# Kernel tuning notes

Measured on AMD Instinct MI355X. Metric: run time of the kernel, lower is better.

## Reference

```python
import jax, jax.numpy as jnp
import numpy as np

N_U, N_M, E, L = 100000, 20000, 2000000, 500000
F_U, F_M, H = 64, 128, 128


def setup_inputs() -> dict:
    key = jax.random.key(0)
    ks = jax.random.split(key, 48)
    p = lambda k, shape: jax.random.normal(k, shape, jnp.float32) * 0.02
    inp = {
        'x_user': jax.random.normal(ks[0], (N_U, F_U), jnp.float32),
        'x_movie': jax.random.normal(ks[1], (N_M, F_M), jnp.float32),
        'edge_index': jnp.stack([jax.random.randint(ks[2], (E,), 0, N_U),
                                 jax.random.randint(ks[3], (E,), 0, N_M)]),
        'edge_label_index': jnp.stack([jax.random.randint(ks[4], (L,), 0, N_U),
                                       jax.random.randint(ks[5], (L,), 0, N_M)]),
        # per-type input projections (LazyLinear)
        'lin_u_W': p(ks[6], (H, F_U)), 'lin_u_b': p(ks[7], (H,)),
        'lin_m_W': p(ks[8], (H, F_M)), 'lin_m_b': p(ks[9], (H,)),
        # BatchNorm (eval mode: running stats)
        'bn_u_g': 1.0 + p(ks[10], (H,)), 'bn_u_b': p(ks[11], (H,)),
        'bn_u_m': p(ks[12], (H,)) * 5.0,
        'bn_u_v': jax.random.uniform(ks[13], (H,), jnp.float32, 0.5, 1.5),
        'bn_m_g': 1.0 + p(ks[14], (H,)), 'bn_m_b': p(ks[15], (H,)),
        'bn_m_m': p(ks[16], (H,)) * 5.0,
        'bn_m_v': jax.random.uniform(ks[17], (H,), jnp.float32, 0.5, 1.5),
        # conv1: SAGEConv per relation (Wl applied to aggregated, Wr to root)
        'c1_um_Wl': p(ks[18], (H, H)), 'c1_um_bl': p(ks[19], (H,)), 'c1_um_Wr': p(ks[20], (H, H)),
        'c1_mu_Wl': p(ks[21], (H, H)), 'c1_mu_bl': p(ks[22], (H,)), 'c1_mu_Wr': p(ks[23], (H, H)),
        # conv2
        'c2_um_Wl': p(ks[24], (H, H)), 'c2_um_bl': p(ks[25], (H,)), 'c2_um_Wr': p(ks[26], (H, H)),
        'c2_mu_Wl': p(ks[27], (H, H)), 'c2_mu_bl': p(ks[28], (H,)), 'c2_mu_Wr': p(ks[29], (H, H)),
        # edge decoder MLP: 2H -> 4H -> 2H -> 1
        'dec_W1': p(ks[30], (4 * H, 2 * H)), 'dec_b1': p(ks[31], (4 * H,)),
        'dec_W2': p(ks[32], (2 * H, 4 * H)), 'dec_b2': p(ks[33], (2 * H,)),
        'dec_W3': p(ks[34], (1, 2 * H)), 'dec_b3': p(ks[35], (1,)),
    }
    return inp


def _bn(x, g, b, m, v):
    return (x - m) * jax.lax.rsqrt(v + 1e-5) * g + b


def _seg_mean(msg, dst, n):
    s = jax.ops.segment_sum(msg, dst, num_segments=n)
    c = jax.ops.segment_sum(jnp.ones((dst.shape[0], 1), msg.dtype), dst, num_segments=n)
    return s / jnp.maximum(c, 1.0)


def _sage(x_src, x_dst, src, dst, Wl, bl, Wr):
    # PyG SAGEConv(aggr='mean'): lin_l(mean of source msgs) + lin_r(x_dst)
    agg = _seg_mean(x_src[src], dst, x_dst.shape[0])
    return agg @ Wl.T + bl + x_dst @ Wr.T


def reference(x_user, x_movie, edge_index, edge_label_index,
              lin_u_W, lin_u_b, lin_m_W, lin_m_b,
              bn_u_g, bn_u_b, bn_u_m, bn_u_v,
              bn_m_g, bn_m_b, bn_m_m, bn_m_v,
              c1_um_Wl, c1_um_bl, c1_um_Wr, c1_mu_Wl, c1_mu_bl, c1_mu_Wr,
              c2_um_Wl, c2_um_bl, c2_um_Wr, c2_mu_Wl, c2_mu_bl, c2_mu_Wr,
              dec_W1, dec_b1, dec_W2, dec_b2, dec_W3, dec_b3):
    u, m = edge_index[0], edge_index[1]
    # per-type projection + BN(eval) + ReLU (Dropout is identity in eval)
    xu = jnp.maximum(_bn(x_user @ lin_u_W.T + lin_u_b, bn_u_g, bn_u_b, bn_u_m, bn_u_v), 0.0)
    xm = jnp.maximum(_bn(x_movie @ lin_m_W.T + lin_m_b, bn_m_g, bn_m_b, bn_m_m, bn_m_v), 0.0)
    # conv1: user->movie and movie->user (HeteroConv mean over 1 relation each)
    xm1 = jnp.maximum(_sage(xu, xm, u, m, c1_um_Wl, c1_um_bl, c1_um_Wr), 0.0)
    xu1 = jnp.maximum(_sage(xm, xu, m, u, c1_mu_Wl, c1_mu_bl, c1_mu_Wr), 0.0)
    # conv2 (no activation after, matches forward)
    zm = _sage(xu1, xm1, u, m, c2_um_Wl, c2_um_bl, c2_um_Wr)
    zu = _sage(xm1, xu1, m, u, c2_mu_Wl, c2_mu_bl, c2_mu_Wr)
    # edge decoder: gather + MLP
    feat = jnp.concatenate([zu[edge_label_index[0]], zm[edge_label_index[1]]], axis=-1)
    h = jnp.maximum(feat @ dec_W1.T + dec_b1, 0.0)
    h = jnp.maximum(h @ dec_W2.T + dec_b2, 0.0)
    return (h @ dec_W3.T + dec_b3)[:, 0]
```

## Files before the change

### kernel.cpp

```cpp
#include <hip/hip_runtime.h>

#define NU 100000
#define NM 20000
#define NE 2000000
#define NL 500000
#define H  128
#define MROW 48

typedef __attribute__((ext_vector_type(8))) short bf16x8;
typedef __attribute__((ext_vector_type(4))) float floatx4;
typedef __attribute__((ext_vector_type(8))) unsigned short u16x8;
typedef __attribute__((ext_vector_type(4))) unsigned short u16x4;

__device__ __forceinline__ unsigned short f2b(float x) {
    union { __bf16 h; unsigned short u; } v;
    v.h = (__bf16)x;
    return v.u;
}
__device__ __forceinline__ float b2f(unsigned short h) {
    union { unsigned u; float f; } v; v.u = ((unsigned)h) << 16;
    return v.f;
}

#define SFCH(r, c)  ((r) * 32 + (((c) + (r)) & 31))
#define SH1CH(r, c) ((r) * 16 + (((c) + (r)) & 15))
#define SH2CH(r, c) ((r) * 64 + (((c) + (r)) & 63))

struct TDesc { const float* s; float* d; int R; int C; };
struct TPack { TDesc t[2]; };

__global__ __launch_bounds__(256) void transpose_all(TPack p) {
    TDesc d = p.t[blockIdx.y];
    int n = d.R * d.C;
    for (int i = blockIdx.x * 256 + threadIdx.x; i < n; i += gridDim.x * 256) {
        int r = i / d.C, c = i - r * d.C;
        d.d[c * d.R + r] = d.s[i];
    }
}

__global__ __launch_bounds__(256) void pack_weights(const float* __restrict__ W1,
                                                    const float* __restrict__ W2,
                                                    unsigned short* __restrict__ W1p,
                                                    unsigned short* __restrict__ W2p) {
    const int n = 512 * 256;
    for (int i = blockIdx.x * 256 + threadIdx.x; i < n; i += gridDim.x * 256) {
        int j = i & 7, lane = (i >> 3) & 63;
        int ln = lane & 15, lq = lane >> 4;
        int kg1 = (i >> 9) & 7,  t1 = i >> 12;
        W1p[i] = f2b(W1[(t1 * 16 + ln) * 256 + kg1 * 32 + lq * 8 + j]);
        int kg2 = (i >> 9) & 15, t2 = i >> 13;
        W2p[i] = f2b(W2[(t2 * 16 + ln) * 512 + kg2 * 32 + lq * 8 + j]);
    }
}

struct SPack { const float* w[8]; };
__global__ __launch_bounds__(256) void pack_sage(SPack sp, unsigned short* __restrict__ out) {
    const int n = 8 * 16384;
    for (int i = blockIdx.x * 256 + threadIdx.x; i < n; i += gridDim.x * 256) {
        int j = i & 7, lane = (i >> 3) & 63;
        int kg = (i >> 9) & 3, t = (i >> 11) & 7, wsel = i >> 14;
        int ln = lane & 15, lq = lane >> 4;
        out[i] = f2b(sp.w[wsel][(t * 16 + ln) * H + kg * 32 + lq * 8 + j]);
    }
}

__global__ __launch_bounds__(256) void deg_kernel(const int* __restrict__ ei,
                                                  int* rp_m, int* rp_u) {
    for (int i = blockIdx.x * 256 + threadIdx.x; i < NE; i += gridDim.x * 256) {
        int u = ei[i], m = ei[NE + i];
        atomicAdd(&rp_u[u + 1], 1);
        atomicAdd(&rp_m[m + 1], 1);
    }
}

__global__ __launch_bounds__(256) void scan_p1(const int* __restrict__ rp_m, int n_m,
                                               const int* __restrict__ rp_u, int n_u,
                                               int* __restrict__ aux) {
    const int arr = blockIdx.y;
    const int* a = arr ? rp_u : rp_m;
    const int n  = arr ? n_u : n_m;
    const int nb = (n + 4095) >> 12;
    const int b  = blockIdx.x;
    if (b >= nb) return;
    __shared__ int s[256];
    const int tid = threadIdx.x;
    int i0 = (b << 12) + tid * 16;
    int run = 0;
#pragma unroll
    for (int i = 0; i < 16; ++i) { int idx = i0 + i; run += (idx < n) ? a[idx] : 0; }
    s[tid] = run;
    __syncthreads();
    for (int off = 128; off > 0; off >>= 1) {
        if (tid < off) s[tid] += s[tid + off];
        __syncthreads();
    }
    if (tid == 0) aux[arr * 32 + b] = s[0];
}

__global__ __launch_bounds__(256) void scan_p2(int* __restrict__ rp_m, int n_m,
                                               int* __restrict__ rp_u, int n_u,
                                               const int* __restrict__ aux) {
    const int arr = blockIdx.y;
    int* a = arr ? rp_u : rp_m;
    const int n  = arr ? n_u : n_m;
    const int nb = (n + 4095) >> 12;
    const int b  = blockIdx.x;
    if (b >= nb) return;
    __shared__ int s[256];
    __shared__ int sc;
    const int tid = threadIdx.x;
    if (tid == 0) {
        int c = 0;
        for (int i = 0; i < b; ++i) c += aux[arr * 32 + i];
        sc = c;
    }
    int i0 = (b << 12) + tid * 16;
    int v[16];
    int run = 0;
#pragma unroll
    for (int i = 0; i < 16; ++i) {
        int idx = i0 + i;
        int x = (idx < n) ? a[idx] : 0;
        run += x; v[i] = run;
    }
    s[tid] = run;
    __syncthreads();
    for (int off = 1; off < 256; off <<= 1) {
        int t = (tid >= off) ? s[tid - off] : 0;
        __syncthreads();
        s[tid] += t;
        __syncthreads();
    }
    int prev = sc + (tid > 0 ? s[tid - 1] : 0);
#pragma unroll
    for (int i = 0; i < 16; ++i) {
        int idx = i0 + i;
        if (idx < n) a[idx] = v[i] + prev;
    }
}

__global__ __launch_bounds__(256) void bucket_kernel(const int* __restrict__ ei,
        const int* __restrict__ rp_m, const int* __restrict__ rp_u,
        int* cur_m, int* cur_u, int* es_m, int* es_u) {
    for (int i = blockIdx.x * 256 + threadIdx.x; i < NE; i += gridDim.x * 256) {
        int u = ei[i], m = ei[NE + i];
        int pm = atomicAdd(&cur_m[m], 1);
        es_m[rp_m[m] + pm] = u;
        int pu = atomicAdd(&cur_u[u], 1);
        es_u[rp_u[u] + pu] = m;
    }
}

template <int K>
__global__ __launch_bounds__(256, 2) void proj_kernel(
        const float* __restrict__ x, const float* __restrict__ Wt,
        const float* __restrict__ lb, const float* __restrict__ g,
        const float* __restrict__ bb, const float* __restrict__ bm,
        const float* __restrict__ bv, unsigned short* __restrict__ out, int N) {
    __shared__ float sA[64 * K];
    const int tid = threadIdx.x;
    const int row0 = blockIdx.x * 64;
    constexpr int F4 = K / 4;
#pragma unroll
    for (int i = 0; i < (64 * F4) / 256; ++i) {
        int idx = tid + i * 256;
        int r = idx / F4, c = idx - r * F4;
        int gr = min(row0 + r, N - 1);
        ((float4*)sA)[idx] = ((const float4*)(x + (size_t)gr * K))[c];
    }
    __syncthreads();
    const int h_t = tid & 31, r_t = tid >> 5;
    float acc[8][4] = {};
#pragma unroll 4
    for (int k = 0; k < K; k += 4) {
        float4 w[4];
#pragma unroll
        for (int kk = 0; kk < 4; ++kk)
            w[kk] = *(const float4*)(Wt + (k + kk) * H + h_t * 4);
#pragma unroll
        for (int rr = 0; rr < 8; ++rr) {
            float4 a = *(const float4*)(sA + (r_t * 8 + rr) * K + k);
            acc[rr][0] += a.x * w[0].x + a.y * w[1].x + a.z * w[2].x + a.w * w[3].x;
            acc[rr][1] += a.x * w[0].y + a.y * w[1].y + a.z * w[2].y + a.w * w[3].y;
            acc[rr][2] += a.x * w[0].z + a.y * w[1].z + a.z * w[2].z + a.w * w[3].z;
            acc[rr][3] += a.x * w[0].w + a.y * w[1].w + a.z * w[2].w + a.w * w[3].w;
        }
    }
    const int h = h_t * 4;
    float4 lb4 = *(const float4*)(lb + h);
    float4 g4  = *(const float4*)(g  + h);
    float4 bb4 = *(const float4*)(bb + h);
    float4 m4  = *(const float4*)(bm + h);
    float4 v4  = *(const float4*)(bv + h);
    float sc[4] = { g4.x * rsqrtf(v4.x + 1e-5f), g4.y * rsqrtf(v4.y + 1e-5f),
                    g4.z * rsqrtf(v4.z + 1e-5f), g4.w * rsqrtf(v4.w + 1e-5f) };
    float lbv[4] = { lb4.x, lb4.y, lb4.z, lb4.w };
    float mv[4]  = { m4.x, m4.y, m4.z, m4.w };
    float bbv[4] = { bb4.x, bb4.y, bb4.z, bb4.w };
#pragma unroll
    for (int rr = 0; rr < 8; ++rr) {
        int gr = row0 + r_t * 8 + rr;
        if (gr < N) {
            u16x4 o;
#pragma unroll
            for (int c = 0; c < 4; ++c)
                o[c] = f2b(fmaxf((acc[rr][c] + lbv[c] - mv[c]) * sc[c] + bbv[c], 0.0f));
            *(u16x4*)(out + (size_t)gr * H + h) = o;
        }
    }
}

__global__ __launch_bounds__(256) void agg_bf16(
        const unsigned short* __restrict__ srcA, const int* __restrict__ esA,
        const int* __restrict__ rpA, unsigned short* __restrict__ outA, int nA,
        const unsigned short* __restrict__ srcB, const int* __restrict__ esB,
        const int* __restrict__ rpB, unsigned short* __restrict__ outB, int nB) {
    int wid = blockIdx.x * 4 + (threadIdx.x >> 6);
    const int lane = threadIdx.x & 63;
    const unsigned short* src; const int* es; const int* rp; unsigned short* out; int n;
    if (wid < nA) { src = srcA; es = esA; rp = rpA; out = outA; n = wid; }
    else {
        wid -= nA;
        if (wid >= nB) return;
        src = srcB; es = esB; rp = rpB; out = outB; n = wid;
    }
    const int start = rp[n], end = rp[n + 1];
    const int cb = (lane & 15) * 8;
    const int ro = lane >> 4;
    float acc[8] = {};
    if (end > start) {
        int j = start;
        for (; j + 16 <= end; j += 16) {
            u16x8 v0 = *(const u16x8*)(src + (size_t)es[j +      ro] * H + cb);
            u16x8 v1 = *(const u16x8*)(src + (size_t)es[j +  4 + ro] * H + cb);
            u16x8 v2 = *(const u16x8*)(src + (size_t)es[j +  8 + ro] * H + cb);
            u16x8 v3 = *(const u16x8*)(src + (size_t)es[j + 12 + ro] * H + cb);
#pragma unroll
            for (int e = 0; e < 8; ++e)
                acc[e] += b2f(v0[e]) + b2f(v1[e]) + b2f(v2[e]) + b2f(v3[e]);
        }
        for (; j + 4 <= end; j += 4) {
            u16x8 v = *(const u16x8*)(src + (size_t)es[j + ro] * H + cb);
#pragma unroll
            for (int e = 0; e < 8; ++e) acc[e] += b2f(v[e]);
        }
        if (j < end) {
            int idx = j + ro;
            int row = es[idx < end ? idx : end - 1];
            float m = (idx < end) ? 1.0f : 0.0f;
            u16x8 v = *(const u16x8*)(src + (size_t)row * H + cb);
#pragma unroll
            for (int e = 0; e < 8; ++e) acc[e] = fmaf(m, b2f(v[e]), acc[e]);
        }
    }
#pragma unroll
    for (int e = 0; e < 8; ++e) {
        acc[e] += __shfl_xor(acc[e], 16);
        acc[e] += __shfl_xor(acc[e], 32);
    }
    float inv = (end > start) ? 1.0f / (float)(end - start) : 0.0f;
    if (ro == 0) {
        u16x8 o;
#pragma unroll
        for (int e = 0; e < 8; ++e) o[e] = f2b(acc[e] * inv);
        *(u16x8*)(out + (size_t)n * H + cb) = o;
    }
}

__global__ __launch_bounds__(256, 4) void sage_mfma(
        const unsigned short* __restrict__ aggA, const unsigned short* __restrict__ xA,
        const unsigned short* __restrict__ WlA, const unsigned short* __restrict__ WrA,
        const float* __restrict__ blA, unsigned short* __restrict__ outA, int NA, int NBLKA,
        const unsigned short* __restrict__ aggB, const unsigned short* __restrict__ xB,
        const unsigned short* __restrict__ WlB, const unsigned short* __restrict__ WrB,
        const float* __restrict__ blB, unsigned short* __restrict__ outB, int NB,
        int relu) {
    __shared__ unsigned short sAg[64 * 16 * 8];
    __shared__ unsigned short sX[64 * 16 * 8];
    const int tid = threadIdx.x;
    const unsigned short *agg, *x, *Wl, *Wr; const float* bl; unsigned short* out;
    int N, row0;
    if ((int)blockIdx.x < NBLKA) {
        agg = aggA; x = xA; Wl = WlA; Wr = WrA; bl = blA; out = outA; N = NA;
        row0 = blockIdx.x * 64;
    } else {
        agg = aggB; x = xB; Wl = WlB; Wr = WrB; bl = blB; out = outB; N = NB;
        row0 = (blockIdx.x - NBLKA) * 64;
    }
#pragma unroll
    for (int i = 0; i < 4; ++i) {
        int idx = tid + i * 256;
        int r = idx >> 4, c = idx & 15;
        int gr = min(row0 + r, N - 1);
        *(u16x8*)(sAg + SH1CH(r, c) * 8) = *(const u16x8*)(agg + (size_t)gr * H + c * 8);
        *(u16x8*)(sX  + SH1CH(r, c) * 8) = *(const u16x8*)(x   + (size_t)gr * H + c * 8);
    }
    __syncthreads();
    const int lane = tid & 63, w = tid >> 6;
    const int ln = lane & 15, lq = lane >> 4;
    floatx4 acc[2][4] = {};
#pragma unroll 2
    for (int kg = 0; kg < 4; ++kg) {
        bf16x8 aA[4], aX[4];
#pragma unroll
        for (int mt = 0; mt < 4; ++mt) {
            aA[mt] = *(const bf16x8*)(sAg + SH1CH(mt * 16 + ln, kg * 4 + lq) * 8);
            aX[mt] = *(const bf16x8*)(sX  + SH1CH(mt * 16 + ln, kg * 4 + lq) * 8);
        }
#pragma unroll
        for (int nt = 0; nt < 2; ++nt) {
            int widx = ((w * 2 + nt) * 4 + kg) * 512 + lane * 8;
            bf16x8 bL = *(const bf16x8*)(Wl + widx);
            bf16x8 bR = *(const bf16x8*)(Wr + widx);
#pragma unroll
            for (int mt = 0; mt < 4; ++mt) {
                acc[nt][mt] = __builtin_amdgcn_mfma_f32_16x16x32_bf16(aA[mt], bL, acc[nt][mt], 0, 0, 0);
                acc[nt][mt] = __builtin_amdgcn_mfma_f32_16x16x32_bf16(aX[mt], bR, acc[nt][mt], 0, 0, 0);
            }
        }
    }
    __syncthreads();
    {
#pragma unroll
        for (int nt = 0; nt < 2; ++nt) {
            int ncol = w * 32 + nt * 16 + ln;
            float bv = bl[ncol];
            int cch = ncol >> 3, coff = ncol & 7;
#pragma unroll
            for (int mt = 0; mt < 4; ++mt)
#pragma unroll
                for (int i = 0; i < 4; ++i) {
                    int row = mt * 16 + lq * 4 + i;
                    float v = acc[nt][mt][i] + bv;
                    if (relu) v = fmaxf(v, 0.0f);
                    sAg[SH1CH(row, cch) * 8 + coff] = f2b(v);
                }
        }
    }
    __syncthreads();
#pragma unroll
    for (int i = 0; i < 4; ++i) {
        int idx = tid + i * 256;
        int r = idx >> 4, c = idx & 15;
        int gr = row0 + r;
        if (gr < N)
            *(u16x8*)(out + (size_t)gr * H + c * 8) = *(const u16x8*)(sAg + SH1CH(r, c) * 8);
    }
}

__global__ __launch_bounds__(512, 4) void decoder_mfma(
        const unsigned short* __restrict__ zu, const unsigned short* __restrict__ zm,
        const int* __restrict__ eli,
        const unsigned short* __restrict__ W1p, const float* __restrict__ b1,
        const unsigned short* __restrict__ W2p, const float* __restrict__ b2,
        const float* __restrict__ W3, const float* __restrict__ b3,
        float* __restrict__ out) {
    __shared__ unsigned short sF[MROW * 32 * 8];
    __shared__ unsigned short sH1[MROW * 64 * 8];
    const int tid = threadIdx.x;
    const int row0 = blockIdx.x * MROW;
    {
        int r = tid >> 3, p = tid & 7;
        if (r < MROW) {
            int rg = min(row0 + r, NL - 1);
            int iu = eli[rg], im = eli[NL + rg];
            const unsigned short* zur = zu + (size_t)iu * H;
            const unsigned short* zmr = zm + (size_t)im * H;
#pragma unroll
            for (int j = 0; j < 4; ++j) {
                int c = p + j * 8;
                const unsigned short* s = (c < 16) ? (zur + c * 8) : (zmr + (c - 16) * 8);
                *(u16x8*)(sF + SFCH(r, c) * 8) = *(const u16x8*)s;
            }
        }
    }
    __syncthreads();
    const int lane = tid & 63, w = tid >> 6;
    const int ln = lane & 15, lq = lane >> 4;
    {
        floatx4 acc1[4][3] = {};
        const unsigned short* w1base = W1p + ((size_t)(w * 4) * 8) * 512 + lane * 8;
        __builtin_amdgcn_s_setprio(1);
#pragma unroll 2
        for (int kg = 0; kg < 8; ++kg) {
            bf16x8 fb[3];
#pragma unroll
            for (int mt = 0; mt < 3; ++mt)
                fb[mt] = *(const bf16x8*)(sF + SFCH(mt * 16 + ln, kg * 4 + lq) * 8);
#pragma unroll
            for (int nt = 0; nt < 4; ++nt) {
                bf16x8 wa = *(const bf16x8*)(w1base + (size_t)(nt * 8 + kg) * 512);
#pragma unroll
                for (int mt = 0; mt < 3; ++mt)
                    acc1[nt][mt] = __builtin_amdgcn_mfma_f32_16x16x32_bf16(wa, fb[mt], acc1[nt][mt], 0, 0, 0);
            }
        }
        __builtin_amdgcn_s_setprio(0);
#pragma unroll
        for (int nt = 0; nt < 4; ++nt) {
            int colbase = w * 64 + nt * 16 + lq * 4;
            float4 bv = *(const float4*)(b1 + colbase);
            int cch = colbase >> 3, coff = colbase & 7;
#pragma unroll
            for (int mt = 0; mt < 3; ++mt) {
                int erow = mt * 16 + ln;
                u16x4 o = { f2b(fmaxf(acc1[nt][mt][0] + bv.x, 0.0f)),
                            f2b(fmaxf(acc1[nt][mt][1] + bv.y, 0.0f)),
                            f2b(fmaxf(acc1[nt][mt][2] + bv.z, 0.0f)),
                            f2b(fmaxf(acc1[nt][mt][3] + bv.w, 0.0f)) };
                *(u16x4*)(sH1 + SH2CH(erow, cch) * 8 + coff) = o;
            }
        }
    }
    __syncthreads();
    floatx4 acc3[2][3] = {};
    {
        const unsigned short* w2base = W2p + ((size_t)(w * 2) * 16) * 512 + lane * 8;
        __builtin_amdgcn_s_setprio(1);
#pragma unroll 2
        for (int kg = 0; kg < 16; ++kg) {
            bf16x8 hb[3];
#pragma unroll
            for (int mt = 0; mt < 3; ++mt)
                hb[mt] = *(const bf16x8*)(sH1 + SH2CH(mt * 16 + ln, kg * 4 + lq) * 8);
#pragma unroll
            for (int nt = 0; nt < 2; ++nt) {
                bf16x8 wa = *(const bf16x8*)(w2base + (size_t)(nt * 16 + kg) * 512);
#pragma unroll
                for (int mt = 0; mt < 3; ++mt)
                    acc3[nt][mt] = __builtin_amdgcn_mfma_f32_16x16x32_bf16(wa, hb[mt], acc3[nt][mt], 0, 0, 0);
            }
        }
        __builtin_amdgcn_s_setprio(0);
    }
    float* sP = (float*)sF;
    {
        float4 w3a = *(const float4*)(W3 + w * 32 + lq * 4);
        float4 w3b = *(const float4*)(W3 + w * 32 + 16 + lq * 4);
        float4 b2a = *(const float4*)(b2 + w * 32 + lq * 4);
        float4 b2b = *(const float4*)(b2 + w * 32 + 16 + lq * 4);
#pragma unroll
        for (int mt = 0; mt < 3; ++mt) {
            float s =
                fmaxf(acc3[0][mt][0] + b2a.x, 0.0f) * w3a.x +
                fmaxf(acc3[0][mt][1] + b2a.y, 0.0f) * w3a.y +
                fmaxf(acc3[0][mt][2] + b2a.z, 0.0f) * w3a.z +
                fmaxf(acc3[0][mt][3] + b2a.w, 0.0f) * w3a.w +
                fmaxf(acc3[1][mt][0] + b2b.x, 0.0f) * w3b.x +
                fmaxf(acc3[1][mt][1] + b2b.y, 0.0f) * w3b.y +
                fmaxf(acc3[1][mt][2] + b2b.z, 0.0f) * w3b.z +
                fmaxf(acc3[1][mt][3] + b2b.w, 0.0f) * w3b.w;
            sP[(mt * 16 + ln) * 36 + w * 4 + lq] = s;
        }
    }
    __syncthreads();
    {
        int r = tid >> 3, p = tid & 7;
        if (r < MROW) {
            float4 v = *(const float4*)(sP + r * 36 + p * 4);
            float sum = v.x + v.y + v.z + v.w;
            sum += __shfl_down(sum, 4, 8);
            sum += __shfl_down(sum, 2, 8);
            sum += __shfl_down(sum, 1, 8);
            if (p == 0 && row0 + r < NL) out[row0 + r] = sum + b3[0];
        }
    }
}

extern "C" void kernel_launch(void* const* d_in, const int* in_sizes, int n_in,
                              void* d_out, int out_size, void* d_ws, size_t ws_size,
                              hipStream_t stream) {
    const float* x_user  = (const float*)d_in[0];
    const float* x_movie = (const float*)d_in[1];
    const int*   ei      = (const int*)d_in[2];
    const int*   eli     = (const int*)d_in[3];
    const float* lin_u_W = (const float*)d_in[4];
    const float* lin_u_b = (const float*)d_in[5];
    const float* lin_m_W = (const float*)d_in[6];
    const float* lin_m_b = (const float*)d_in[7];
    const float* bn_u_g  = (const float*)d_in[8];
    const float* bn_u_b  = (const float*)d_in[9];
    const float* bn_u_m  = (const float*)d_in[10];
    const float* bn_u_v  = (const float*)d_in[11];
    const float* bn_m_g  = (const float*)d_in[12];
    const float* bn_m_b  = (const float*)d_in[13];
    const float* bn_m_m  = (const float*)d_in[14];
    const float* bn_m_v  = (const float*)d_in[15];
    const float* c1_um_Wl = (const float*)d_in[16];
    const float* c1_um_bl = (const float*)d_in[17];
    const float* c1_um_Wr = (const float*)d_in[18];
    const float* c1_mu_Wl = (const float*)d_in[19];
    const float* c1_mu_bl = (const float*)d_in[20];
    const float* c1_mu_Wr = (const float*)d_in[21];
    const float* c2_um_Wl = (const float*)d_in[22];
    const float* c2_um_bl = (const float*)d_in[23];
    const float* c2_um_Wr = (const float*)d_in[24];
    const float* c2_mu_Wl = (const float*)d_in[25];
    const float* c2_mu_bl = (const float*)d_in[26];
    const float* c2_mu_Wr = (const float*)d_in[27];
    const float* dec_W1 = (const float*)d_in[28];
    const float* dec_b1 = (const float*)d_in[29];
    const float* dec_W2 = (const float*)d_in[30];
    const float* dec_b2 = (const float*)d_in[31];
    const float* dec_W3 = (const float*)d_in[32];
    const float* dec_b3 = (const float*)d_in[33];

    char* base = (char*)d_ws;
    size_t off = 0;
    auto alloc = [&](size_t bytes) -> char* {
        char* p = base + off;
        off += (bytes + 255) & ~(size_t)255;
        return p;
    };
    unsigned short* xu_b  = (unsigned short*)alloc((size_t)NU * H * 2);
    unsigned short* xm_b  = (unsigned short*)alloc((size_t)NM * H * 2);
    unsigned short* xu1_b = (unsigned short*)alloc((size_t)NU * H * 2);
    unsigned short* xm1_b = (unsigned short*)alloc((size_t)NM * H * 2);
    unsigned short* aggu  = (unsigned short*)alloc((size_t)NU * H * 2);
    unsigned short* aggm  = (unsigned short*)alloc((size_t)NM * H * 2);
    float* wt_u = (float*)alloc((size_t)64 * H * 4);
    float* wt_m = (float*)alloc((size_t)H * H * 4);
    unsigned short* wsg = (unsigned short*)alloc((size_t)8 * 16384 * 2);
    unsigned short* w1p = (unsigned short*)alloc((size_t)512 * 256 * 2);
    unsigned short* w2p = (unsigned short*)alloc((size_t)256 * 512 * 2);
    int* rp_m  = (int*)alloc((size_t)(NM + 1) * 4);
    int* rp_u  = (int*)alloc((size_t)(NU + 1) * 4);
    int* cur_m = (int*)alloc((size_t)NM * 4);
    int* cur_u = (int*)alloc((size_t)NU * 4);
    int* es_m  = (int*)alloc((size_t)NE * 4);
    int* es_u  = (int*)alloc((size_t)NE * 4);
    int* scan_aux = (int*)alloc((size_t)64 * 4);
    unsigned short* zu = xu_b;
    unsigned short* zm = xm_b;

    hipMemsetAsync(rp_m, 0, (size_t)((char*)es_m - (char*)rp_m), stream);

    TPack tp;
    tp.t[0] = { lin_u_W, wt_u, H, 64 };
    tp.t[1] = { lin_m_W, wt_m, H, H };
    transpose_all<<<dim3(64, 2), 256, 0, stream>>>(tp);
    pack_weights<<<256, 256, 0, stream>>>(dec_W1, dec_W2, w1p, w2p);
    SPack sp;
    sp.w[0] = c1_um_Wl; sp.w[1] = c1_um_Wr; sp.w[2] = c1_mu_Wl; sp.w[3] = c1_mu_Wr;
    sp.w[4] = c2_um_Wl; sp.w[5] = c2_um_Wr; sp.w[6] = c2_mu_Wl; sp.w[7] = c2_mu_Wr;
    pack_sage<<<128, 256, 0, stream>>>(sp, wsg);
    const unsigned short* W_c1um_l = wsg + 0 * 16384;
    const unsigned short* W_c1um_r = wsg + 1 * 16384;
    const unsigned short* W_c1mu_l = wsg + 2 * 16384;
    const unsigned short* W_c1mu_r = wsg + 3 * 16384;
    const unsigned short* W_c2um_l = wsg + 4 * 16384;
    const unsigned short* W_c2um_r = wsg + 5 * 16384;
    const unsigned short* W_c2mu_l = wsg + 6 * 16384;
    const unsigned short* W_c2mu_r = wsg + 7 * 16384;

    deg_kernel<<<2048, 256, 0, stream>>>(ei, rp_m, rp_u);
    scan_p1<<<dim3(25, 2), 256, 0, stream>>>(rp_m, NM + 1, rp_u, NU + 1, scan_aux);
    scan_p2<<<dim3(25, 2), 256, 0, stream>>>(rp_m, NM + 1, rp_u, NU + 1, scan_aux);
    bucket_kernel<<<2048, 256, 0, stream>>>(ei, rp_m, rp_u, cur_m, cur_u, es_m, es_u);

    proj_kernel<64><<<(NU + 63) / 64, 256, 0, stream>>>(
        x_user, wt_u, lin_u_b, bn_u_g, bn_u_b, bn_u_m, bn_u_v, xu_b, NU);
    proj_kernel<128><<<(NM + 63) / 64, 256, 0, stream>>>(
        x_movie, wt_m, lin_m_b, bn_m_g, bn_m_b, bn_m_m, bn_m_v, xm_b, NM);

    const int AGG_BLOCKS = (NM + NU + 3) / 4;
    const int NBLK_M = (NM + 63) / 64, NBLK_U = (NU + 63) / 64;

    agg_bf16<<<AGG_BLOCKS, 256, 0, stream>>>(xu_b, es_m, rp_m, aggm, NM,
                                             xm_b, es_u, rp_u, aggu, NU);
    sage_mfma<<<NBLK_M + NBLK_U, 256, 0, stream>>>(
        aggm, xm_b, W_c1um_l, W_c1um_r, c1_um_bl, xm1_b, NM, NBLK_M,
        aggu, xu_b, W_c1mu_l, W_c1mu_r, c1_mu_bl, xu1_b, NU, 1);
    agg_bf16<<<AGG_BLOCKS, 256, 0, stream>>>(xu1_b, es_m, rp_m, aggm, NM,
                                             xm1_b, es_u, rp_u, aggu, NU);
    sage_mfma<<<NBLK_M + NBLK_U, 256, 0, stream>>>(
        aggm, xm1_b, W_c2um_l, W_c2um_r, c2_um_bl, zm, NM, NBLK_M,
        aggu, xu1_b, W_c2mu_l, W_c2mu_r, c2_mu_bl, zu, NU, 0);

    decoder_mfma<<<(NL + MROW - 1) / MROW, 512, 0, stream>>>(
        zu, zm, eli, w1p, dec_b1, w2p, dec_b2, dec_W3, dec_b3, (float*)d_out);
}
```

Baseline: 1.116 ms.

## Fuse prep kernels, record atomic slot in degree pass, merge bucket with projection

The weight transpose and packing kernels are merged with the degree-count kernel into one launch, and each edge's atomicAdd result is saved as its slot within its bucket. The bucket pass then writes edges directly using that saved slot, with no second round of atomics. It runs in the same launch as the user and movie projections. This cuts the number of kernel launches and the contended atomics, at the cost of an extra 16 MB of slot arrays stored in the aggu buffer. It also removes the s_setprio hints from the decoder MFMA loops.

```diff
diff --git a/kernel.cpp b/kernel.cpp
--- a/kernel.cpp
+++ b/kernel.cpp
@@ -26,50 +26,53 @@
 #define SH1CH(r, c) ((r) * 16 + (((c) + (r)) & 15))
 #define SH2CH(r, c) ((r) * 64 + (((c) + (r)) & 63))
 
-struct TDesc { const float* s; float* d; int R; int C; };
-struct TPack { TDesc t[2]; };
-
-__global__ __launch_bounds__(256) void transpose_all(TPack p) {
-    TDesc d = p.t[blockIdx.y];
-    int n = d.R * d.C;
-    for (int i = blockIdx.x * 256 + threadIdx.x; i < n; i += gridDim.x * 256) {
-        int r = i / d.C, c = i - r * d.C;
-        d.d[c * d.R + r] = d.s[i];
-    }
-}
-
-__global__ __launch_bounds__(256) void pack_weights(const float* __restrict__ W1,
-                                                    const float* __restrict__ W2,
-                                                    unsigned short* __restrict__ W1p,
-                                                    unsigned short* __restrict__ W2p) {
-    const int n = 512 * 256;
-    for (int i = blockIdx.x * 256 + threadIdx.x; i < n; i += gridDim.x * 256) {
-        int j = i & 7, lane = (i >> 3) & 63;
-        int ln = lane & 15, lq = lane >> 4;
-        int kg1 = (i >> 9) & 7,  t1 = i >> 12;
-        W1p[i] = f2b(W1[(t1 * 16 + ln) * 256 + kg1 * 32 + lq * 8 + j]);
-        int kg2 = (i >> 9) & 15, t2 = i >> 13;
-        W2p[i] = f2b(W2[(t2 * 16 + ln) * 512 + kg2 * 32 + lq * 8 + j]);
-    }
-}
-
-struct SPack { const float* w[8]; };
-__global__ __launch_bounds__(256) void pack_sage(SPack sp, unsigned short* __restrict__ out) {
-    const int n = 8 * 16384;
-    for (int i = blockIdx.x * 256 + threadIdx.x; i < n; i += gridDim.x * 256) {
-        int j = i & 7, lane = (i >> 3) & 63;
-        int kg = (i >> 9) & 3, t = (i >> 11) & 7, wsel = i >> 14;
-        int ln = lane & 15, lq = lane >> 4;
-        out[i] = f2b(sp.w[wsel][(t * 16 + ln) * H + kg * 32 + lq * 8 + j]);
-    }
-}
-
-__global__ __launch_bounds__(256) void deg_kernel(const int* __restrict__ ei,
-                                                  int* rp_m, int* rp_u) {
-    for (int i = blockIdx.x * 256 + threadIdx.x; i < NE; i += gridDim.x * 256) {
-        int u = ei[i], m = ei[NE + i];
-        atomicAdd(&rp_u[u + 1], 1);
-        atomicAdd(&rp_m[m + 1], 1);
+struct PrepArgs {
+    const float* luW; float* wtu;
+    const float* lmW; float* wtm;
+    const float* W1; const float* W2;
+    unsigned short* W1p; unsigned short* W2p;
+    const float* sw[8]; unsigned short* wsg;
+    const int* ei; int* rp_m; int* rp_u; int* pos_m; int* pos_u;
+};
+
+__global__ __launch_bounds__(256) void prep1(PrepArgs a) {
+    const int b = blockIdx.x, tid = threadIdx.x;
+    if (b < 64) {
+        const int n = H * 64;
+        for (int i = b * 256 + tid; i < n; i += 64 * 256) {
+            int r = i >> 6, c = i & 63;
+            a.wtu[c * H + r] = a.luW[i];
+        }
+    } else if (b < 128) {
+        const int n = H * H;
+        for (int i = (b - 64) * 256 + tid; i < n; i += 64 * 256) {
+            int r = i >> 7, c = i & 127;
+            a.wtm[c * H + r] = a.lmW[i];
+        }
+    } else if (b < 384) {
+        const int n = 512 * 256;
+        for (int i = (b - 128) * 256 + tid; i < n; i += 256 * 256) {
+            int j = i & 7, lane = (i >> 3) & 63;
+            int ln = lane & 15, lq = lane >> 4;
+            int kg1 = (i >> 9) & 7,  t1 = i >> 12;
+            a.W1p[i] = f2b(a.W1[(t1 * 16 + ln) * 256 + kg1 * 32 + lq * 8 + j]);
+            int kg2 = (i >> 9) & 15, t2 = i >> 13;
+            a.W2p[i] = f2b(a.W2[(t2 * 16 + ln) * 512 + kg2 * 32 + lq * 8 + j]);
+        }
+    } else if (b < 512) {
+        const int n = 8 * 16384;
+        for (int i = (b - 384) * 256 + tid; i < n; i += 128 * 256) {
+            int j = i & 7, lane = (i >> 3) & 63;
+            int kg = (i >> 9) & 3, t = (i >> 11) & 7, wsel = i >> 14;
+            int ln = lane & 15, lq = lane >> 4;
+            a.wsg[i] = f2b(a.sw[wsel][(t * 16 + ln) * H + kg * 32 + lq * 8 + j]);
+        }
+    } else {
+        for (int i = (b - 512) * 256 + tid; i < NE; i += 2048 * 256) {
+            int u = a.ei[i], m = a.ei[NE + i];
+            a.pos_u[i] = atomicAdd(&a.rp_u[u + 1], 1);
+            a.pos_m[i] = atomicAdd(&a.rp_m[m + 1], 1);
+        }
     }
 }
 
@@ -139,27 +142,15 @@
     }
 }
 
-__global__ __launch_bounds__(256) void bucket_kernel(const int* __restrict__ ei,
-        const int* __restrict__ rp_m, const int* __restrict__ rp_u,
-        int* cur_m, int* cur_u, int* es_m, int* es_u) {
-    for (int i = blockIdx.x * 256 + threadIdx.x; i < NE; i += gridDim.x * 256) {
-        int u = ei[i], m = ei[NE + i];
-        int pm = atomicAdd(&cur_m[m], 1);
-        es_m[rp_m[m] + pm] = u;
-        int pu = atomicAdd(&cur_u[u], 1);
-        es_u[rp_u[u] + pu] = m;
-    }
-}
-
 template <int K>
-__global__ __launch_bounds__(256, 2) void proj_kernel(
+__device__ __forceinline__ void proj_body(
         const float* __restrict__ x, const float* __restrict__ Wt,
         const float* __restrict__ lb, const float* __restrict__ g,
         const float* __restrict__ bb, const float* __restrict__ bm,
-        const float* __restrict__ bv, unsigned short* __restrict__ out, int N) {
-    __shared__ float sA[64 * K];
+        const float* __restrict__ bv, unsigned short* __restrict__ out, int N,
+        int blk, float* sA) {
     const int tid = threadIdx.x;
-    const int row0 = blockIdx.x * 64;
+    const int row0 = blk * 64;
     constexpr int F4 = K / 4;
 #pragma unroll
     for (int i = 0; i < (64 * F4) / 256; ++i) {
@@ -207,6 +198,36 @@
                 o[c] = f2b(fmaxf((acc[rr][c] + lbv[c] - mv[c]) * sc[c] + bbv[c], 0.0f));
             *(u16x4*)(out + (size_t)gr * H + h) = o;
         }
+    }
+}
+
+struct PBArgs {
+    const int* ei; const int* rp_m; const int* rp_u;
+    const int* pos_m; const int* pos_u; int* es_m; int* es_u;
+    const float* xu; const float* wtu;
+    const float* lub; const float* bug; const float* bub; const float* bum; const float* buv;
+    unsigned short* xu_b;
+    const float* xm; const float* wtm;
+    const float* lmb; const float* bmg; const float* bmb; const float* bmm; const float* bmv;
+    unsigned short* xm_b;
+    int nbu;
+};
+
+__global__ __launch_bounds__(256, 2) void projbucket(PBArgs a) {
+    __shared__ float sA[64 * H];
+    const int b = blockIdx.x;
+    if (b < 2048) {
+        for (int i = b * 256 + threadIdx.x; i < NE; i += 2048 * 256) {
+            int u = a.ei[i], m = a.ei[NE + i];
+            a.es_m[a.rp_m[m] + a.pos_m[i]] = u;
+            a.es_u[a.rp_u[u] + a.pos_u[i]] = m;
+        }
+    } else if (b < 2048 + a.nbu) {
+        proj_body<64>(a.xu, a.wtu, a.lub, a.bug, a.bub, a.bum, a.buv, a.xu_b, NU,
+                      b - 2048, sA);
+    } else {
+        proj_body<128>(a.xm, a.wtm, a.lmb, a.bmg, a.bmb, a.bmm, a.bmv, a.xm_b, NM,
+                       b - 2048 - a.nbu, sA);
     }
 }
 
@@ -380,7 +401,6 @@
     {
         floatx4 acc1[4][3] = {};
         const unsigned short* w1base = W1p + ((size_t)(w * 4) * 8) * 512 + lane * 8;
-        __builtin_amdgcn_s_setprio(1);
 #pragma unroll 2
         for (int kg = 0; kg < 8; ++kg) {
             bf16x8 fb[3];
@@ -395,7 +415,6 @@
                     acc1[nt][mt] = __builtin_amdgcn_mfma_f32_16x16x32_bf16(wa, fb[mt], acc1[nt][mt], 0, 0, 0);
             }
         }
-        __builtin_amdgcn_s_setprio(0);
 #pragma unroll
         for (int nt = 0; nt < 4; ++nt) {
             int colbase = w * 64 + nt * 16 + lq * 4;
@@ -416,7 +435,6 @@
     floatx4 acc3[2][3] = {};
     {
         const unsigned short* w2base = W2p + ((size_t)(w * 2) * 16) * 512 + lane * 8;
-        __builtin_amdgcn_s_setprio(1);
 #pragma unroll 2
         for (int kg = 0; kg < 16; ++kg) {
             bf16x8 hb[3];
@@ -431,7 +449,6 @@
                     acc3[nt][mt] = __builtin_amdgcn_mfma_f32_16x16x32_bf16(wa, hb[mt], acc3[nt][mt], 0, 0, 0);
             }
         }
-        __builtin_amdgcn_s_setprio(0);
     }
     float* sP = (float*)sF;
     {
@@ -525,25 +542,42 @@
     unsigned short* w2p = (unsigned short*)alloc((size_t)256 * 512 * 2);
     int* rp_m  = (int*)alloc((size_t)(NM + 1) * 4);
     int* rp_u  = (int*)alloc((size_t)(NU + 1) * 4);
-    int* cur_m = (int*)alloc((size_t)NM * 4);
-    int* cur_u = (int*)alloc((size_t)NU * 4);
     int* es_m  = (int*)alloc((size_t)NE * 4);
     int* es_u  = (int*)alloc((size_t)NE * 4);
     int* scan_aux = (int*)alloc((size_t)64 * 4);
     unsigned short* zu = xu_b;
     unsigned short* zm = xm_b;
+    int* pos_m = (int*)aggu;
+    int* pos_u = pos_m + NE;
 
     hipMemsetAsync(rp_m, 0, (size_t)((char*)es_m - (char*)rp_m), stream);
 
-    TPack tp;
-    tp.t[0] = { lin_u_W, wt_u, H, 64 };
-    tp.t[1] = { lin_m_W, wt_m, H, H };
-    transpose_all<<<dim3(64, 2), 256, 0, stream>>>(tp);
-    pack_weights<<<256, 256, 0, stream>>>(dec_W1, dec_W2, w1p, w2p);
-    SPack sp;
-    sp.w[0] = c1_um_Wl; sp.w[1] = c1_um_Wr; sp.w[2] = c1_mu_Wl; sp.w[3] = c1_mu_Wr;
-    sp.w[4] = c2_um_Wl; sp.w[5] = c2_um_Wr; sp.w[6] = c2_mu_Wl; sp.w[7] = c2_mu_Wr;
-    pack_sage<<<128, 256, 0, stream>>>(sp, wsg);
+    PrepArgs pa;
+    pa.luW = lin_u_W; pa.wtu = wt_u;
+    pa.lmW = lin_m_W; pa.wtm = wt_m;
+    pa.W1 = dec_W1; pa.W2 = dec_W2; pa.W1p = w1p; pa.W2p = w2p;
+    pa.sw[0] = c1_um_Wl; pa.sw[1] = c1_um_Wr; pa.sw[2] = c1_mu_Wl; pa.sw[3] = c1_mu_Wr;
+    pa.sw[4] = c2_um_Wl; pa.sw[5] = c2_um_Wr; pa.sw[6] = c2_mu_Wl; pa.sw[7] = c2_mu_Wr;
+    pa.wsg = wsg;
+    pa.ei = ei; pa.rp_m = rp_m; pa.rp_u = rp_u; pa.pos_m = pos_m; pa.pos_u = pos_u;
+    prep1<<<2560, 256, 0, stream>>>(pa);
+
+    scan_p1<<<dim3(25, 2), 256, 0, stream>>>(rp_m, NM + 1, rp_u, NU + 1, scan_aux);
+    scan_p2<<<dim3(25, 2), 256, 0, stream>>>(rp_m, NM + 1, rp_u, NU + 1, scan_aux);
+
+    const int NBU = (NU + 63) / 64, NBM = (NM + 63) / 64;
+    PBArgs pb;
+    pb.ei = ei; pb.rp_m = rp_m; pb.rp_u = rp_u;
+    pb.pos_m = pos_m; pb.pos_u = pos_u; pb.es_m = es_m; pb.es_u = es_u;
+    pb.xu = x_user; pb.wtu = wt_u;
+    pb.lub = lin_u_b; pb.bug = bn_u_g; pb.bub = bn_u_b; pb.bum = bn_u_m; pb.buv = bn_u_v;
+    pb.xu_b = xu_b;
+    pb.xm = x_movie; pb.wtm = wt_m;
+    pb.lmb = lin_m_b; pb.bmg = bn_m_g; pb.bmb = bn_m_b; pb.bmm = bn_m_m; pb.bmv = bn_m_v;
+    pb.xm_b = xm_b;
+    pb.nbu = NBU;
+    projbucket<<<2048 + NBU + NBM, 256, 0, stream>>>(pb);
+
     const unsigned short* W_c1um_l = wsg + 0 * 16384;
     const unsigned short* W_c1um_r = wsg + 1 * 16384;
     const unsigned short* W_c1mu_l = wsg + 2 * 16384;
@@ -552,16 +586,6 @@
     const unsigned short* W_c2um_r = wsg + 5 * 16384;
     const unsigned short* W_c2mu_l = wsg + 6 * 16384;
     const unsigned short* W_c2mu_r = wsg + 7 * 16384;
-
-    deg_kernel<<<2048, 256, 0, stream>>>(ei, rp_m, rp_u);
-    scan_p1<<<dim3(25, 2), 256, 0, stream>>>(rp_m, NM + 1, rp_u, NU + 1, scan_aux);
-    scan_p2<<<dim3(25, 2), 256, 0, stream>>>(rp_m, NM + 1, rp_u, NU + 1, scan_aux);
-    bucket_kernel<<<2048, 256, 0, stream>>>(ei, rp_m, rp_u, cur_m, cur_u, es_m, es_u);
-
-    proj_kernel<64><<<(NU + 63) / 64, 256, 0, stream>>>(
-        x_user, wt_u, lin_u_b, bn_u_g, bn_u_b, bn_u_m, bn_u_v, xu_b, NU);
-    proj_kernel<128><<<(NM + 63) / 64, 256, 0, stream>>>(
-        x_movie, wt_m, lin_m_b, bn_m_g, bn_m_b, bn_m_m, bn_m_v, xm_b, NM);
 
     const int AGG_BLOCKS = (NM + NU + 3) / 4;
     const int NBLK_M = (NM + 63) / 64, NBLK_U = (NU + 63) / 64;
```

Result: faster. 948.0 us, median of 2 (-15.0%).
